# Optimization experiments

Measured on AMD Instinct MI355X. Metric: run time of the kernel, lower is better.

The kernel has to match this reference:

```python
import jax, jax.numpy as jnp
import numpy as np

N, P, C_IN, C_OUT, C_FEAT = 100000, 32, 4, 64, 9
BN_EPS = 1e-3


def setup_inputs() -> dict:
    key = jax.random.key(0)
    k1, k2, k3, k4 = jax.random.split(key, 4)
    voxels = jax.random.normal(k1, (N, P, C_IN), dtype=jnp.float32)
    num_points_per_voxel = jax.random.randint(k2, (N,), 1, P + 1, dtype=jnp.int32)
    voxel_centers = jax.random.normal(k3, (N, 2), dtype=jnp.float32)
    W = jax.random.normal(k4, (C_OUT, C_FEAT), dtype=jnp.float32) * (1.0 / np.sqrt(C_FEAT))
    gamma = jnp.ones((C_OUT,), dtype=jnp.float32)
    beta = jnp.zeros((C_OUT,), dtype=jnp.float32)
    return {"voxels": voxels, "num_points_per_voxel": num_points_per_voxel,
            "voxel_centers": voxel_centers, "W": W, "gamma": gamma, "beta": beta}


def reference(voxels, num_points_per_voxel, voxel_centers, W, gamma, beta):
    npts = num_points_per_voxel.astype(voxels.dtype)[:, None, None]  # [N,1,1]
    # cluster offset: per-pillar mean of xyz
    points_mean = voxels[:, :, :3].sum(axis=1, keepdims=True) / npts  # [N,1,3]
    f_cluster = voxels[:, :, :3] - points_mean                        # [N,P,3]
    # center offset: xy minus Cartesian voxel center
    f_center = voxels[:, :, :2] - voxel_centers[:, None, :]           # [N,P,2]
    features = jnp.concatenate([voxels, f_cluster, f_center], axis=-1)  # [N,P,9]
    # zero out padded points
    mask = num_points_per_voxel[:, None] > jnp.arange(P, dtype=jnp.int32)[None, :]
    features = features * mask[:, :, None].astype(features.dtype)
    # PFNLayer (last_layer=True): linear(no bias) -> BN(batch stats) -> relu -> max over points
    x = jnp.einsum('npc,oc->npo', features, W)  # [N,P,64]
    mean = x.mean(axis=(0, 1))
    var = ((x - mean) ** 2).mean(axis=(0, 1))   # biased var, as torch BN training
    x = (x - mean) * jax.lax.rsqrt(var + BN_EPS) * gamma + beta
    x = jax.nn.relu(x)
    return x.max(axis=1)  # [N,64]
```

## Files before the change

kernel.cpp:

```cpp
#include <hip/hip_runtime.h>
#include <math.h>

#define N_PILLARS 100000
#define P_PTS 32
#define BN_EPS 1e-3f


__global__ __launch_bounds__(256) void pfn_stats(
    const float* __restrict__ vox,
    const int*   __restrict__ npts,
    const float* __restrict__ ctr,
    const float* __restrict__ W,
    float*       __restrict__ gsums,
    float4*      __restrict__ means)
{
    __shared__ float4 sv[4][32];
    __shared__ float  red[2][4][64];

    const int tid  = threadIdx.x;
    const int wave = tid >> 6, lane = tid & 63;
    const int o = lane;

    float w[9];
#pragma unroll
    for (int c = 0; c < 9; ++c) w[c] = W[o * 9 + c];
    const float Wc0 = w[0] + w[4] + w[7];
    const float Wc1 = w[1] + w[5] + w[8];
    const float Wc2 = w[2] + w[6];
    const float Wc3 = w[3];

    float s1 = 0.f, s2 = 0.f;
    const int stride = gridDim.x * 4;
    for (int n = blockIdx.x * 4 + wave; n < N_PILLARS; n += stride) {
        const float2* src = (const float2*)(vox + (size_t)n * 128);
        ((float2*)&sv[wave][lane >> 1])[lane & 1] = src[lane];

        float4 pv = sv[wave][lane & 31];
        float sx = pv.x, sy = pv.y, sz = pv.z;
#pragma unroll
        for (int m = 1; m < 32; m <<= 1) {
            sx += __shfl_xor(sx, m);
            sy += __shfl_xor(sy, m);
            sz += __shfl_xor(sz, m);
        }
        const int   np  = npts[n];
        const float inv = 1.0f / (float)np;
        const float mx = sx * inv, my = sy * inv, mz = sz * inv;
        const float cx = ctr[n * 2 + 0], cyv = ctr[n * 2 + 1];
        const float t = -(mx * w[4] + my * w[5] + mz * w[6] + cx * w[7] + cyv * w[8]);

        for (int p = 0; p < np; ++p) {
            float4 v = sv[wave][p];
            float  x = fmaf(v.x, Wc0, t);
            x = fmaf(v.y, Wc1, x);
            x = fmaf(v.z, Wc2, x);
            x = fmaf(v.w, Wc3, x);
            s1 += x;
            s2 = fmaf(x, x, s2);
        }
        if (lane == 0) means[n] = make_float4(mx, my, mz, 0.f);
    }

    red[0][wave][lane] = s1;
    red[1][wave][lane] = s2;
    __syncthreads();
    if (wave == 0) {
        float a = red[0][0][lane] + red[0][1][lane] + red[0][2][lane] + red[0][3][lane];
        float b = red[1][0][lane] + red[1][1][lane] + red[1][2][lane] + red[1][3][lane];
        atomicAdd(&gsums[lane], a);
        atomicAdd(&gsums[64 + lane], b);
    }
}

__global__ void pfn_scale(const float* __restrict__ gsums,
                          const float* __restrict__ gamma,
                          const float* __restrict__ beta,
                          float* __restrict__ sb)
{
    int o = threadIdx.x;
    if (o < 64) {
        const float invNP = 1.0f / (float)(N_PILLARS * P_PTS);
        float mean = gsums[o] * invNP;
        float var  = gsums[64 + o] * invNP - mean * mean;
        float sc   = gamma[o] * rsqrtf(var + BN_EPS);
        sb[o]      = sc;
        sb[64 + o] = beta[o] - mean * sc;
    }
}

__global__ __launch_bounds__(256) void pfn_final(
    const float*  __restrict__ vox,
    const int*    __restrict__ npts,
    const float*  __restrict__ ctr,
    const float*  __restrict__ W,
    const float4* __restrict__ means,
    const float*  __restrict__ sb,
    float*        __restrict__ out)
{
    __shared__ float4 sv[4][32];

    const int tid  = threadIdx.x;
    const int wave = tid >> 6, lane = tid & 63;
    const int o = lane;

    const float w4 = W[o * 9 + 4], w5 = W[o * 9 + 5], w6 = W[o * 9 + 6];
    const float w7 = W[o * 9 + 7], w8 = W[o * 9 + 8];
    const float Wc0 = W[o * 9 + 0] + w4 + w7;
    const float Wc1 = W[o * 9 + 1] + w5 + w8;
    const float Wc2 = W[o * 9 + 2] + w6;
    const float Wc3 = W[o * 9 + 3];
    const float sc = sb[o], bs = sb[64 + o];

    const int stride = gridDim.x * 4;
    for (int n = blockIdx.x * 4 + wave; n < N_PILLARS; n += stride) {
        const int np = npts[n];
        const int p  = lane >> 1;
        if (p < np)
            ((float2*)&sv[wave][p])[lane & 1] =
                ((const float2*)(vox + (size_t)n * 128))[lane];

        const float4 m  = means[n];
        const float  cx = ctr[n * 2 + 0], cyv = ctr[n * 2 + 1];
        const float  t  = -(m.x * w4 + m.y * w5 + m.z * w6 + cx * w7 + cyv * w8);

        float hi = -INFINITY, lo = INFINITY;
        for (int q = 0; q < np; ++q) {
            float4 v = sv[wave][q];
            float  x = fmaf(v.x, Wc0, t);
            x = fmaf(v.y, Wc1, x);
            x = fmaf(v.z, Wc2, x);
            x = fmaf(v.w, Wc3, x);
            hi = fmaxf(hi, x);
            lo = fminf(lo, x);
        }
        if (np < P_PTS) { hi = fmaxf(hi, 0.f); lo = fminf(lo, 0.f); }

        const float mm = (sc >= 0.f) ? hi : lo;
        out[(size_t)n * 64 + o] = fmaxf(0.f, fmaf(mm, sc, bs));
    }
}

extern "C" void kernel_launch(void* const* d_in, const int* in_sizes, int n_in,
                              void* d_out, int out_size, void* d_ws, size_t ws_size,
                              hipStream_t stream) {
    const float* voxels  = (const float*)d_in[0];
    const int*   npts    = (const int*)d_in[1];
    const float* centers = (const float*)d_in[2];
    const float* W       = (const float*)d_in[3];
    const float* gamma   = (const float*)d_in[4];
    const float* beta    = (const float*)d_in[5];
    float* out = (float*)d_out;

    float*  gsums = (float*)d_ws;
    float*  sb    = (float*)d_ws + 128;
    float4* means = (float4*)((char*)d_ws + 1024);

    hipMemsetAsync(d_ws, 0, 512, stream);
    pfn_stats<<<1024, 256, 0, stream>>>(voxels, npts, centers, W, gsums, means);
    pfn_scale<<<1, 64, 0, stream>>>(gsums, gamma, beta, sb);
    pfn_final<<<2048, 256, 0, stream>>>(voxels, npts, centers, W, means, sb, out);
}
```

Before: 179.7 us.

## Process two pillars per wave with float4 loads and hoist per-pillar offset

Each wave now handles a pair of pillars, loading all 64 float4 points in a single coalesced float4 access instead of float2 per pillar. The per-pillar constant term is pulled out of the inner loops: stats are computed from raw sums and corrected algebraically, and min/max are shifted by the offset afterwards. Inner loops are unrolled, launch bounds request higher occupancy, and the stats grid is doubled. This cuts shuffle, load and loop overhead per pillar. It risks more float cancellation in the variance expansion and more register pressure from handling two pillars at once.

```diff
diff --git a/kernel.cpp b/kernel.cpp
--- a/kernel.cpp
+++ b/kernel.cpp
@@ -2,11 +2,12 @@
 #include <math.h>
 
 #define N_PILLARS 100000
+#define N_PAIRS   (N_PILLARS / 2)
 #define P_PTS 32
 #define BN_EPS 1e-3f
 
 
-__global__ __launch_bounds__(256) void pfn_stats(
+__global__ __launch_bounds__(256, 8) void pfn_stats(
     const float* __restrict__ vox,
     const int*   __restrict__ npts,
     const float* __restrict__ ctr,
@@ -14,12 +15,12 @@
     float*       __restrict__ gsums,
     float4*      __restrict__ means)
 {
-    __shared__ float4 sv[4][32];
+    __shared__ float4 sv[4][64];
     __shared__ float  red[2][4][64];
 
     const int tid  = threadIdx.x;
     const int wave = tid >> 6, lane = tid & 63;
-    const int o = lane;
+    const int o = lane, pl = lane & 31;
 
     float w[9];
 #pragma unroll
@@ -30,35 +31,57 @@
     const float Wc3 = w[3];
 
     float s1 = 0.f, s2 = 0.f;
-    const int stride = gridDim.x * 4;
-    for (int n = blockIdx.x * 4 + wave; n < N_PILLARS; n += stride) {
-        const float2* src = (const float2*)(vox + (size_t)n * 128);
-        ((float2*)&sv[wave][lane >> 1])[lane & 1] = src[lane];
-
-        float4 pv = sv[wave][lane & 31];
-        float sx = pv.x, sy = pv.y, sz = pv.z;
+    const int wid = blockIdx.x * 4 + wave, nw = gridDim.x * 4;
+    for (int pr = wid; pr < N_PAIRS; pr += nw) {
+        const int n0 = pr * 2;
+        const float4 mine = ((const float4*)(vox + (size_t)n0 * 128))[lane];
+        const int   np0 = npts[n0],  np1 = npts[n0 + 1];
+        const float2 c0 = ((const float2*)ctr)[n0];
+        const float2 c1 = ((const float2*)ctr)[n0 + 1];
+        sv[wave][lane] = mine;
+
+        float sx = mine.x, sy = mine.y, sz = mine.z;
 #pragma unroll
         for (int m = 1; m < 32; m <<= 1) {
             sx += __shfl_xor(sx, m);
             sy += __shfl_xor(sy, m);
             sz += __shfl_xor(sz, m);
         }
-        const int   np  = npts[n];
-        const float inv = 1.0f / (float)np;
-        const float mx = sx * inv, my = sy * inv, mz = sz * inv;
-        const float cx = ctr[n * 2 + 0], cyv = ctr[n * 2 + 1];
-        const float t = -(mx * w[4] + my * w[5] + mz * w[6] + cx * w[7] + cyv * w[8]);
-
-        for (int p = 0; p < np; ++p) {
+        const float sx0 = __shfl(sx, pl),      sy0 = __shfl(sy, pl),      sz0 = __shfl(sz, pl);
+        const float sx1 = __shfl(sx, pl | 32), sy1 = __shfl(sy, pl | 32), sz1 = __shfl(sz, pl | 32);
+
+        const float i0 = 1.0f / (float)np0, i1 = 1.0f / (float)np1;
+        const float t0 = -(sx0 * i0 * w[4] + sy0 * i0 * w[5] + sz0 * i0 * w[6]
+                           + c0.x * w[7] + c0.y * w[8]);
+        const float t1 = -(sx1 * i1 * w[4] + sy1 * i1 * w[5] + sz1 * i1 * w[6]
+                           + c1.x * w[7] + c1.y * w[8]);
+
+        float a1 = 0.f, a2 = 0.f;
+#pragma unroll 4
+        for (int p = 0; p < np0; ++p) {
             float4 v = sv[wave][p];
-            float  x = fmaf(v.x, Wc0, t);
-            x = fmaf(v.y, Wc1, x);
-            x = fmaf(v.z, Wc2, x);
-            x = fmaf(v.w, Wc3, x);
-            s1 += x;
-            s2 = fmaf(x, x, s2);
-        }
-        if (lane == 0) means[n] = make_float4(mx, my, mz, 0.f);
+            float  y = fmaf(v.x, Wc0, v.y * Wc1);
+            y = fmaf(v.z, Wc2, y);
+            y = fmaf(v.w, Wc3, y);
+            a1 += y; a2 = fmaf(y, y, a2);
+        }
+        float b1 = 0.f, b2 = 0.f;
+#pragma unroll 4
+        for (int p = 0; p < np1; ++p) {
+            float4 v = sv[wave][32 + p];
+            float  y = fmaf(v.x, Wc0, v.y * Wc1);
+            y = fmaf(v.z, Wc2, y);
+            y = fmaf(v.w, Wc3, y);
+            b1 += y; b2 = fmaf(y, y, b2);
+        }
+        s1 += a1 + (float)np0 * t0 + b1 + (float)np1 * t1;
+        s2 += a2 + t0 * (2.f * a1 + (float)np0 * t0)
+            + b2 + t1 * (2.f * b1 + (float)np1 * t1);
+
+        if (lane == 0) {
+            means[n0]     = make_float4(sx0 * i0, sy0 * i0, sz0 * i0, 0.f);
+            means[n0 + 1] = make_float4(sx1 * i1, sy1 * i1, sz1 * i1, 0.f);
+        }
     }
 
     red[0][wave][lane] = s1;
@@ -88,7 +111,7 @@
     }
 }
 
-__global__ __launch_bounds__(256) void pfn_final(
+__global__ __launch_bounds__(256, 8) void pfn_final(
     const float*  __restrict__ vox,
     const int*    __restrict__ npts,
     const float*  __restrict__ ctr,
@@ -97,11 +120,11 @@
     const float*  __restrict__ sb,
     float*        __restrict__ out)
 {
-    __shared__ float4 sv[4][32];
+    __shared__ float4 sv[4][64];
 
     const int tid  = threadIdx.x;
     const int wave = tid >> 6, lane = tid & 63;
-    const int o = lane;
+    const int o = lane, pl = lane & 31, half = lane >> 5;
 
     const float w4 = W[o * 9 + 4], w5 = W[o * 9 + 5], w6 = W[o * 9 + 6];
     const float w7 = W[o * 9 + 7], w8 = W[o * 9 + 8];
@@ -111,32 +134,48 @@
     const float Wc3 = W[o * 9 + 3];
     const float sc = sb[o], bs = sb[64 + o];
 
-    const int stride = gridDim.x * 4;
-    for (int n = blockIdx.x * 4 + wave; n < N_PILLARS; n += stride) {
-        const int np = npts[n];
-        const int p  = lane >> 1;
-        if (p < np)
-            ((float2*)&sv[wave][p])[lane & 1] =
-                ((const float2*)(vox + (size_t)n * 128))[lane];
-
-        const float4 m  = means[n];
-        const float  cx = ctr[n * 2 + 0], cyv = ctr[n * 2 + 1];
-        const float  t  = -(m.x * w4 + m.y * w5 + m.z * w6 + cx * w7 + cyv * w8);
-
-        float hi = -INFINITY, lo = INFINITY;
-        for (int q = 0; q < np; ++q) {
+    const int wid = blockIdx.x * 4 + wave, nw = gridDim.x * 4;
+    for (int pr = wid; pr < N_PAIRS; pr += nw) {
+        const int n0 = pr * 2;
+        const int np0 = npts[n0], np1 = npts[n0 + 1];
+        const int npm = half ? np1 : np0;
+        if (pl < npm)
+            sv[wave][lane] = ((const float4*)(vox + (size_t)n0 * 128))[lane];
+
+        const float4 m0 = means[n0], m1 = means[n0 + 1];
+        const float2 c0 = ((const float2*)ctr)[n0];
+        const float2 c1 = ((const float2*)ctr)[n0 + 1];
+        const float t0 = -(m0.x * w4 + m0.y * w5 + m0.z * w6 + c0.x * w7 + c0.y * w8);
+        const float t1 = -(m1.x * w4 + m1.y * w5 + m1.z * w6 + c1.x * w7 + c1.y * w8);
+
+        float h0 = -INFINITY, l0 = INFINITY;
+#pragma unroll 4
+        for (int q = 0; q < np0; ++q) {
             float4 v = sv[wave][q];
-            float  x = fmaf(v.x, Wc0, t);
-            x = fmaf(v.y, Wc1, x);
-            x = fmaf(v.z, Wc2, x);
-            x = fmaf(v.w, Wc3, x);
-            hi = fmaxf(hi, x);
-            lo = fminf(lo, x);
-        }
-        if (np < P_PTS) { hi = fmaxf(hi, 0.f); lo = fminf(lo, 0.f); }
-
-        const float mm = (sc >= 0.f) ? hi : lo;
-        out[(size_t)n * 64 + o] = fmaxf(0.f, fmaf(mm, sc, bs));
+            float  y = fmaf(v.x, Wc0, v.y * Wc1);
+            y = fmaf(v.z, Wc2, y);
+            y = fmaf(v.w, Wc3, y);
+            h0 = fmaxf(h0, y); l0 = fminf(l0, y);
+        }
+        float h1 = -INFINITY, l1 = INFINITY;
+#pragma unroll 4
+        for (int q = 0; q < np1; ++q) {
+            float4 v = sv[wave][32 + q];
+            float  y = fmaf(v.x, Wc0, v.y * Wc1);
+            y = fmaf(v.z, Wc2, y);
+            y = fmaf(v.w, Wc3, y);
+            h1 = fmaxf(h1, y); l1 = fminf(l1, y);
+        }
+
+        float hi0 = h0 + t0, lo0 = l0 + t0;
+        float hi1 = h1 + t1, lo1 = l1 + t1;
+        if (np0 < P_PTS) { hi0 = fmaxf(hi0, 0.f); lo0 = fminf(lo0, 0.f); }
+        if (np1 < P_PTS) { hi1 = fmaxf(hi1, 0.f); lo1 = fminf(lo1, 0.f); }
+
+        const float mm0 = (sc >= 0.f) ? hi0 : lo0;
+        const float mm1 = (sc >= 0.f) ? hi1 : lo1;
+        out[(size_t)n0 * 64 + o]       = fmaxf(0.f, fmaf(mm0, sc, bs));
+        out[(size_t)(n0 + 1) * 64 + o] = fmaxf(0.f, fmaf(mm1, sc, bs));
     }
 }
 
@@ -156,7 +195,7 @@
     float4* means = (float4*)((char*)d_ws + 1024);
 
     hipMemsetAsync(d_ws, 0, 512, stream);
-    pfn_stats<<<1024, 256, 0, stream>>>(voxels, npts, centers, W, gsums, means);
+    pfn_stats<<<2048, 256, 0, stream>>>(voxels, npts, centers, W, gsums, means);
     pfn_scale<<<1, 64, 0, stream>>>(gsums, gamma, beta, sb);
     pfn_final<<<2048, 256, 0, stream>>>(voxels, npts, centers, W, means, sb, out);
 }
```

New measurement: 183.7 us. +2.2%, slower.
